# Performance work log

Measured on AMD Instinct MI355X. Metric: run time of the kernel, lower is better.

The kernel has to match this reference:

```python
import jax, jax.numpy as jnp
import numpy as np
from jax import lax

T, B, D, H, K, A = 256, 512, 128, 50, 5, 4


def setup_inputs() -> dict:
    key = jax.random.key(0)
    ks = jax.random.split(key, 12)
    s = 0.05
    return {
        "x": jax.random.normal(ks[0], (T, B, D), dtype=jnp.float32),
        "W_in": jax.random.normal(ks[1], (H, D), dtype=jnp.float32) * s,
        "b_in": jax.random.normal(ks[2], (H,), dtype=jnp.float32) * s,
        "W_ctx": jax.random.normal(ks[3], (H, 2 * H), dtype=jnp.float32) * s,
        "b_ctx": jax.random.normal(ks[4], (H,), dtype=jnp.float32) * s,
        "W_key": jax.random.normal(ks[5], (K, H), dtype=jnp.float32) * s,
        "b_key": jax.random.normal(ks[6], (K,), dtype=jnp.float32) * s,
        "W_q": jax.random.normal(ks[7], (K, H), dtype=jnp.float32) * s,
        "b_q": jax.random.normal(ks[8], (K,), dtype=jnp.float32) * s,
        "first_context": jax.random.normal(ks[9], (H,), dtype=jnp.float32) * s,
        "W_act": jax.random.normal(ks[10], (A, H), dtype=jnp.float32) * s,
        "b_act": jax.random.normal(ks[11], (A,), dtype=jnp.float32) * s,
    }


def reference(x, W_in, b_in, W_ctx, b_ctx, W_key, b_key, W_q, b_q,
              first_context, W_act, b_act):
    # Unrolls the torch module's per-step forward() over T steps with a
    # growing attention context (horizon=-1 => attend to full history).
    Tn, Bn, _ = x.shape
    Hn = W_in.shape[0]
    Kn = W_key.shape[0]
    neg_inf = jnp.float32(-1e30)

    c0 = jnp.broadcast_to(first_context[None, :], (Bn, Hn))  # [B,H]
    ctx_buf = jnp.zeros((Tn + 1, Bn, Hn), x.dtype).at[0].set(c0)
    key_buf = jnp.zeros((Tn + 1, Bn, Kn), x.dtype).at[0].set(c0 @ W_key.T + b_key)
    step_ids = jnp.arange(Tn + 1)[:, None]  # [T+1,1]

    def step(carry, xt):
        ctx_buf, key_buf, prev_c, t = carry
        h = jax.nn.relu(xt @ W_in.T + b_in)                           # [B,H]
        c = jax.nn.relu(jnp.concatenate([prev_c, h], axis=1) @ W_ctx.T + b_ctx)
        ctx_buf = ctx_buf.at[t + 1].set(c)
        key_buf = key_buf.at[t + 1].set(c @ W_key.T + b_key)
        q = c @ W_q.T + b_q                                           # [B,K]
        scores = jnp.einsum('tbk,bk->tb', key_buf, q)                 # [T+1,B]
        scores = jnp.where(step_ids <= t + 1, scores, neg_inf)
        attn = jax.nn.softmax(scores, axis=0)                         # over history
        w = jnp.einsum('tb,tbh->bh', attn, ctx_buf)                   # [B,H]
        actions = w @ W_act.T + b_act                                 # [B,A]
        return (ctx_buf, key_buf, c, t + 1), actions

    _, actions = lax.scan(step, (ctx_buf, key_buf, c0, jnp.int32(0)), x)
    return actions  # [T,B,A]
```

## Files before the change

### kernel.cpp

```cpp
#include <hip/hip_runtime.h>

#define TT 256
#define BB 512
#define DD 128
#define HH 50
#define KK 5
#define AA 4
#define NROW 131072
#define GST 52
#define KQS 260

#define R50(X) X(0) X(1) X(2) X(3) X(4) X(5) X(6) X(7) X(8) X(9) \
  X(10) X(11) X(12) X(13) X(14) X(15) X(16) X(17) X(18) X(19) \
  X(20) X(21) X(22) X(23) X(24) X(25) X(26) X(27) X(28) X(29) \
  X(30) X(31) X(32) X(33) X(34) X(35) X(36) X(37) X(38) X(39) \
  X(40) X(41) X(42) X(43) X(44) X(45) X(46) X(47) X(48) X(49)

typedef _Float16 half4 __attribute__((ext_vector_type(4)));
typedef float f32x4 __attribute__((ext_vector_type(4)));

__global__ void k0_prep(const float* __restrict__ W_in,
                        const float* __restrict__ W_ctx,
                        const float* __restrict__ W_key,
                        const float* __restrict__ W_q,
                        const float* __restrict__ b_key,
                        const float* __restrict__ b_q,
                        float* __restrict__ WHT,
                        float* __restrict__ WK2T, float* __restrict__ bias2) {
  int i = blockIdx.x * 256 + threadIdx.x;
  if (i < HH * 52) {
    int j = i / 52, h = i % 52;
    WHT[i] = (h < HH) ? W_ctx[h * (2 * HH) + HH + j] : 0.f;
  }
  if (i < HH * 64) {
    int j = i >> 6, l = i & 63;
    float v = 0.f;
    if (l < HH) v = W_ctx[l * (2 * HH) + j];
    else if (l < HH + KK) v = W_key[(l - HH) * HH + j];
    else if (l < HH + 2 * KK) v = W_q[(l - HH - KK) * HH + j];
    WK2T[i] = v;
  }
  if (i < 64) {
    float bv = 0.f;
    if (i >= HH && i < HH + KK) bv = b_key[i - HH];
    else if (i >= HH + KK && i < HH + 2 * KK) bv = b_q[i - HH - KK];
    bias2[i] = bv;
  }
}

__global__ __launch_bounds__(256, 2) void k1_mfma(
    const float* __restrict__ x, const float* __restrict__ W_in,
    const float* __restrict__ WHT, const float* __restrict__ b_in,
    const float* __restrict__ b_ctx, float* __restrict__ g) {
  const int lane = threadIdx.x & 63;
  const int wave = threadIdx.x >> 6;
  const int lrow = lane & 15, lgrp = lane >> 4;

#define WA1D(m, kk)                                                     \
  half4 wa1_##m##_##kk;                                                 \
  {                                                                     \
    const int hh = 16 * (m) + lrow;                                     \
    const int j0 = 16 * (kk) + 4 * lgrp;                                \
    const bool v = (hh < HH);                                           \
    const float* p = W_in + (size_t)(v ? hh : 0) * DD + j0;             \
    wa1_##m##_##kk[0] = (_Float16)(v ? p[0] : 0.f);                     \
    wa1_##m##_##kk[1] = (_Float16)(v ? p[1] : 0.f);                     \
    wa1_##m##_##kk[2] = (_Float16)(v ? p[2] : 0.f);                     \
    wa1_##m##_##kk[3] = (_Float16)(v ? p[3] : 0.f);                     \
  }
  WA1D(0, 0) WA1D(0, 1) WA1D(0, 2) WA1D(0, 3)
  WA1D(0, 4) WA1D(0, 5) WA1D(0, 6) WA1D(0, 7)
  WA1D(1, 0) WA1D(1, 1) WA1D(1, 2) WA1D(1, 3)
  WA1D(1, 4) WA1D(1, 5) WA1D(1, 6) WA1D(1, 7)
  WA1D(2, 0) WA1D(2, 1) WA1D(2, 2) WA1D(2, 3)
  WA1D(2, 4) WA1D(2, 5) WA1D(2, 6) WA1D(2, 7)
  WA1D(3, 0) WA1D(3, 1) WA1D(3, 2) WA1D(3, 3)
  WA1D(3, 4) WA1D(3, 5) WA1D(3, 6) WA1D(3, 7)

#define WA2D(m, kk)                                                     \
  half4 wa2_##m##_##kk;                                                 \
  {                                                                     \
    const int gg = 16 * (m) + lrow;                                     \
    const int h0 = 16 * (kk) + 4 * lgrp;                                \
    wa2_##m##_##kk[0] = (_Float16)((gg < HH && h0 + 0 < HH) ? WHT[(h0 + 0) * 52 + gg] : 0.f); \
    wa2_##m##_##kk[1] = (_Float16)((gg < HH && h0 + 1 < HH) ? WHT[(h0 + 1) * 52 + gg] : 0.f); \
    wa2_##m##_##kk[2] = (_Float16)((gg < HH && h0 + 2 < HH) ? WHT[(h0 + 2) * 52 + gg] : 0.f); \
    wa2_##m##_##kk[3] = (_Float16)((gg < HH && h0 + 3 < HH) ? WHT[(h0 + 3) * 52 + gg] : 0.f); \
  }
  WA2D(0, 0) WA2D(0, 1) WA2D(0, 2) WA2D(0, 3)
  WA2D(1, 0) WA2D(1, 1) WA2D(1, 2) WA2D(1, 3)
  WA2D(2, 0) WA2D(2, 1) WA2D(2, 2) WA2D(2, 3)
  WA2D(3, 0) WA2D(3, 1) WA2D(3, 2) WA2D(3, 3)

#define BDEF(m, r)                                                      \
  const float bin_##m##_##r =                                           \
      (16 * (m) + 4 * lgrp + (r) < HH) ? b_in[16 * (m) + 4 * lgrp + (r)] : 0.f; \
  const float bct_##m##_##r =                                           \
      (16 * (m) + 4 * lgrp + (r) < HH) ? b_ctx[16 * (m) + 4 * lgrp + (r)] : 0.f;
  BDEF(0, 0) BDEF(0, 1) BDEF(0, 2) BDEF(0, 3)
  BDEF(1, 0) BDEF(1, 1) BDEF(1, 2) BDEF(1, 3)
  BDEF(2, 0) BDEF(2, 1) BDEF(2, 2) BDEF(2, 3)
  BDEF(3, 0) BDEF(3, 1) BDEF(3, 2) BDEF(3, 3)

  const f32x4 zf = {0.f, 0.f, 0.f, 0.f};

#pragma unroll 1
  for (int it = 0; it < 4; ++it) {
    const int tile = (blockIdx.x * 4 + wave) * 4 + it;
    const int row = tile * 16 + lrow;
    const float* __restrict__ xr = x + (size_t)row * DD + 4 * lgrp;

#define XLD(kk)                                                         \
  half4 xb##kk;                                                         \
  {                                                                     \
    const float4 xv = *reinterpret_cast<const float4*>(xr + 16 * kk);   \
    xb##kk[0] = (_Float16)xv.x;                                         \
    xb##kk[1] = (_Float16)xv.y;                                         \
    xb##kk[2] = (_Float16)xv.z;                                         \
    xb##kk[3] = (_Float16)xv.w;                                         \
  }
    XLD(0) XLD(1) XLD(2) XLD(3) XLD(4) XLD(5) XLD(6) XLD(7)

    f32x4 d10 = zf, d11 = zf, d12 = zf, d13 = zf;
#define MM1(kk)                                                              \
  d10 = __builtin_amdgcn_mfma_f32_16x16x16f16(wa1_0_##kk, xb##kk, d10, 0, 0, 0); \
  d11 = __builtin_amdgcn_mfma_f32_16x16x16f16(wa1_1_##kk, xb##kk, d11, 0, 0, 0); \
  d12 = __builtin_amdgcn_mfma_f32_16x16x16f16(wa1_2_##kk, xb##kk, d12, 0, 0, 0); \
  d13 = __builtin_amdgcn_mfma_f32_16x16x16f16(wa1_3_##kk, xb##kk, d13, 0, 0, 0);
    MM1(0) MM1(1) MM1(2) MM1(3) MM1(4) MM1(5) MM1(6) MM1(7)

#define HBD(k)                                                    \
  half4 hb##k;                                                    \
  hb##k[0] = (_Float16)fmaxf(d1##k[0] + bin_##k##_0, 0.f);        \
  hb##k[1] = (_Float16)fmaxf(d1##k[1] + bin_##k##_1, 0.f);        \
  hb##k[2] = (_Float16)fmaxf(d1##k[2] + bin_##k##_2, 0.f);        \
  hb##k[3] = (_Float16)fmaxf(d1##k[3] + bin_##k##_3, 0.f);
    HBD(0) HBD(1) HBD(2) HBD(3)

    f32x4 d20 = zf, d21 = zf, d22 = zf, d23 = zf;
#define MM2(kk)                                                              \
  d20 = __builtin_amdgcn_mfma_f32_16x16x16f16(wa2_0_##kk, hb##kk, d20, 0, 0, 0); \
  d21 = __builtin_amdgcn_mfma_f32_16x16x16f16(wa2_1_##kk, hb##kk, d21, 0, 0, 0); \
  d22 = __builtin_amdgcn_mfma_f32_16x16x16f16(wa2_2_##kk, hb##kk, d22, 0, 0, 0); \
  d23 = __builtin_amdgcn_mfma_f32_16x16x16f16(wa2_3_##kk, hb##kk, d23, 0, 0, 0);
    MM2(0) MM2(1) MM2(2) MM2(3)

    float* __restrict__ gr =
        g + ((size_t)(row & (BB - 1)) * TT + (row >> 9)) * GST;
    *reinterpret_cast<float4*>(gr + 4 * lgrp) =
        make_float4(d20[0] + bct_0_0, d20[1] + bct_0_1, d20[2] + bct_0_2,
                    d20[3] + bct_0_3);
    *reinterpret_cast<float4*>(gr + 16 + 4 * lgrp) =
        make_float4(d21[0] + bct_1_0, d21[1] + bct_1_1, d21[2] + bct_1_2,
                    d21[3] + bct_1_3);
    *reinterpret_cast<float4*>(gr + 32 + 4 * lgrp) =
        make_float4(d22[0] + bct_2_0, d22[1] + bct_2_1, d22[2] + bct_2_2,
                    d22[3] + bct_2_3);
    if (lgrp == 0) {
      *reinterpret_cast<float4*>(gr + 48) =
          make_float4(d23[0] + bct_3_0, d23[1] + bct_3_1, 0.f, 0.f);
    }
  }
}

__global__ __launch_bounds__(64) void k2_rec(
    const float* __restrict__ g, const float* __restrict__ WK2T,
    const float* __restrict__ bias2, const float* __restrict__ first_context,
    float* __restrict__ ctxg, float* __restrict__ kqg) {
  __shared__ __align__(16) float c_lds[64];
  const int b = blockIdx.x;
  const int lane = threadIdx.x;

#define WDECL(j)                            \
  float w##j = WK2T[(j) * 64 + lane];       \
  asm volatile("" : "+v"(w##j));
  R50(WDECL)
  const float wz = 0.f;
  const float bias = bias2[lane];

  const float c0v = (lane < HH) ? first_context[lane] : 0.f;
  c_lds[lane] = (lane < HH) ? c0v : 0.f;
  if (lane < HH) ctxg[((size_t)b * 257 + 0) * HH + lane] = c0v;

  const int gslot = (lane < GST) ? lane : (GST - 1);
  const float* __restrict__ gbp = g + (size_t)b * TT * GST + gslot;
  float gq0 = gbp[0 * GST];
  float gq1 = gbp[1 * GST];
  float gq2 = gbp[2 * GST];
  float gq3 = gbp[3 * GST];

  const bool iskq = (lane >= HH && lane < HH + 2 * KK);
  float* __restrict__ kqrow =
      kqg + ((size_t)b * 10 + (iskq ? lane - HH : 0)) * KQS;

#define KQ(J, wa, wb, wc, wd)                                            \
  {                                                                      \
    const float4 cq = *reinterpret_cast<const float4*>(&c_lds[J]);       \
    acc0 = fmaf(wa, cq.x, acc0);                                         \
    acc1 = fmaf(wb, cq.y, acc1);                                         \
    acc2 = fmaf(wc, cq.z, acc2);                                         \
    acc3 = fmaf(wd, cq.w, acc3);                                         \
  }
#define DOT50R                                                           \
  float acc0 = 0.f, acc1 = 0.f, acc2 = 0.f, acc3 = 0.f;                  \
  KQ(0, w0, w1, w2, w3) KQ(4, w4, w5, w6, w7)                            \
  KQ(8, w8, w9, w10, w11) KQ(12, w12, w13, w14, w15)                     \
  KQ(16, w16, w17, w18, w19) KQ(20, w20, w21, w22, w23)                  \
  KQ(24, w24, w25, w26, w27) KQ(28, w28, w29, w30, w31)                  \
  KQ(32, w32, w33, w34, w35) KQ(36, w36, w37, w38, w39)                  \
  KQ(40, w40, w41, w42, w43) KQ(44, w44, w45, w46, w47)                  \
  KQ(48, w48, w49, wz, wz)                                               \
  const float acc = (acc0 + acc1) + (acc2 + acc3);

#define BODY(RR, GQ)                                                     \
  {                                                                      \
    const int t = tg4 + RR;                                              \
    DOT50R                                                               \
    kqa##RR = acc + bias;                                                \
    const float cn = fmaxf(acc + GQ, 0.f);                               \
    GQ = gbp[(size_t)min(t + 4, TT - 1) * GST];                          \
    if (lane < HH) {                                                     \
      ctxg[((size_t)b * 257 + (t + 1)) * HH + lane] = cn;                \
      c_lds[lane] = cn;                                                  \
    }                                                                    \
  }

#pragma unroll 1
  for (int tg4 = 0; tg4 < TT; tg4 += 4) {
    float kqa0, kqa1, kqa2, kqa3;
    BODY(0, gq0) BODY(1, gq1) BODY(2, gq2) BODY(3, gq3)
    if (iskq) {
      *reinterpret_cast<float4*>(kqrow + tg4) =
          make_float4(kqa0, kqa1, kqa2, kqa3);
    }
  }

  {
    DOT50R
    if (iskq) kqrow[TT] = acc + bias;
  }
}

__global__ __launch_bounds__(256, 4) void k3_attn(
    const float* __restrict__ ctxg, const float* __restrict__ kqg,
    const float* __restrict__ W_act, const float* __restrict__ b_act,
    float* __restrict__ out) {
  __shared__ __align__(16) float ct[64 * 66];
  __shared__ __align__(16) float k_l[16 * 68];
  __shared__ __align__(16) float o_l[64 * 66];
  __shared__ float su_l[64];

  const int tid = threadIdx.x;
  const int bid = blockIdx.x;
  const int chunk = 3 - (bid >> 9);
  const int b = bid & 511;
  const int tbase = chunk * 64;
  const int nst = min(tbase + 66, 257);
  const int ntiles = (nst + 63) >> 6;
  const int wave = tid >> 6;
  const int lane = tid & 63;
  const int lrow = lane & 15;
  const int lgrp = lane >> 4;
  const int tw = tbase + wave * 16;

  for (int i = tid; i < 11 * 68; i += 256) k_l[5 * 68 + i] = 0.f;

  half4 qf;
#pragma unroll
  for (int i = 0; i < 4; ++i) {
    const int k = 4 * lgrp + i;
    qf[i] = (_Float16)((k < KK)
                           ? kqg[((size_t)b * 10 + 5 + k) * KQS + tw + lrow + 1]
                           : 0.f);
  }

  const f32x4 zf = {0.f, 0.f, 0.f, 0.f};
  f32x4 acc0 = zf, acc1 = zf, acc2 = zf, acc3 = zf;
  float su = 0.f;

#pragma unroll 1
  for (int tile = 0; tile < ntiles; ++tile) {
    __syncthreads();
    {
      const int r = tid >> 2;
      const int c0 = (tid & 3) * 16;
      const int srow = tile * 64 + r;
      const float* src = ctxg + ((size_t)b * 257 + srow) * HH;
      const bool sv = (srow < nst);
#pragma unroll
      for (int u = 0; u < 8; ++u) {
        const int c = c0 + u * 2;
        float2 v = make_float2(0.f, 0.f);
        if (sv && c < HH) v = *reinterpret_cast<const float2*>(src + c);
        *reinterpret_cast<float2*>(&ct[r * 66 + c]) = v;
      }
    }
    {
      for (int i = tid; i < KK * 64; i += 256) {
        const int k = i >> 6, sl = i & 63;
        const int s = tile * 64 + sl;
        k_l[k * 68 + sl] =
            (s <= TT) ? kqg[((size_t)b * 10 + k) * KQS + s] : 0.f;
      }
    }
    __syncthreads();

    if (tile * 64 <= tw + 16) {
#pragma unroll 1
      for (int su16 = 0; su16 < 4; ++su16) {
        const int sb = tile * 64 + su16 * 16;
        if (sb > tw + 16) break;

        half4 kf;
#pragma unroll
        for (int i = 0; i < 4; ++i)
          kf[i] = (_Float16)k_l[(4 * lgrp + i) * 68 + su16 * 16 + lrow];

        const f32x4 sc =
            __builtin_amdgcn_mfma_f32_16x16x16f16(kf, qf, zf, 0, 0, 0);

        half4 pa;
#pragma unroll
        for (int r = 0; r < 4; ++r) {
          const int s = sb + 4 * lgrp + r;
          const float p = (s <= tw + lrow + 1) ? __expf(sc[r]) : 0.f;
          su += p;
          pa[r] = (_Float16)p;
        }

        const int vbase = su16 * 16 + 4 * lgrp;
#define PVHT(HT, ACC)                                                     \
  {                                                                       \
    half4 vf;                                                             \
    vf[0] = (_Float16)ct[(vbase + 0) * 66 + lrow + 16 * HT];              \
    vf[1] = (_Float16)ct[(vbase + 1) * 66 + lrow + 16 * HT];              \
    vf[2] = (_Float16)ct[(vbase + 2) * 66 + lrow + 16 * HT];              \
    vf[3] = (_Float16)ct[(vbase + 3) * 66 + lrow + 16 * HT];              \
    ACC = __builtin_amdgcn_mfma_f32_16x16x16f16(pa, vf, ACC, 0, 0, 0);    \
  }
        PVHT(0, acc0) PVHT(1, acc1) PVHT(2, acc2) PVHT(3, acc3)
      }
    }
  }

  su += __shfl_xor(su, 16, 64);
  su += __shfl_xor(su, 32, 64);
  if (lane < 16) su_l[wave * 16 + lane] = su;

#pragma unroll
  for (int r = 0; r < 4; ++r) {
    const int trow = wave * 16 + 4 * lgrp + r;
    o_l[trow * 66 + lrow + 0] = acc0[r];
    o_l[trow * 66 + lrow + 16] = acc1[r];
    o_l[trow * 66 + lrow + 32] = acc2[r];
    o_l[trow * 66 + lrow + 48] = acc3[r];
  }
  __syncthreads();

  {
    const int tl = tid >> 2;
    const int a = tid & 3;
    const float inv = 1.f / su_l[tl];
    const float* orow = &o_l[tl * 66];
    const float* wrow = W_act + a * HH;
    float s0 = 0.f, s1 = 0.f;
#pragma unroll
    for (int h = 0; h < HH; h += 2) {
      s0 = fmaf(orow[h], wrow[h], s0);
      s1 = fmaf(orow[h + 1], wrow[h + 1], s1);
    }
    out[((size_t)(tbase + tl) * BB + b) * AA + a] =
        fmaf(s0 + s1, inv, b_act[a]);
  }
}

extern "C" void kernel_launch(void* const* d_in, const int* in_sizes, int n_in,
                              void* d_out, int out_size, void* d_ws,
                              size_t ws_size, hipStream_t stream) {
  const float* x = (const float*)d_in[0];
  const float* W_in = (const float*)d_in[1];
  const float* b_in = (const float*)d_in[2];
  const float* W_ctx = (const float*)d_in[3];
  const float* b_ctx = (const float*)d_in[4];
  const float* W_key = (const float*)d_in[5];
  const float* b_key = (const float*)d_in[6];
  const float* W_q = (const float*)d_in[7];
  const float* b_q = (const float*)d_in[8];
  const float* fc = (const float*)d_in[9];
  const float* W_act = (const float*)d_in[10];
  const float* b_act = (const float*)d_in[11];
  float* out = (float*)d_out;
  float* ws = (float*)d_ws;

  float* WHT = ws;
  float* WK2T = ws + 4096;
  float* bias2 = ws + 8128;
  float* g = ws + 8192;
  float* ctxg = g + (size_t)NROW * GST + 64;
  float* kqg = ctxg + (size_t)BB * 257 * HH;

  hipLaunchKernelGGL(k0_prep, dim3(26), dim3(256), 0, stream, W_in, W_ctx,
                     W_key, W_q, b_key, b_q, WHT, WK2T, bias2);
  hipLaunchKernelGGL(k1_mfma, dim3(512), dim3(256), 0, stream, x, W_in, WHT,
                     b_in, b_ctx, g);
  hipLaunchKernelGGL(k2_rec, dim3(512), dim3(64), 0, stream, g, WK2T, bias2,
                     fc, ctxg, kqg);
  hipLaunchKernelGGL(k3_attn, dim3(2048), dim3(256), 0, stream, ctxg, kqg,
                     W_act, b_act, out);
}
```

Before: 151.0 us.

## Store gate preactivations as fp16, pad context rows to 64, deepen prefetch

The first stage now writes its per-step context preactivations as half-precision values in a 64-wide padded layout instead of fp32 with stride 52. This halves the intermediate traffic and lets every lane of the recurrent kernel load without clamping. The recurrence stores contexts in 64-float rows without a lane guard, unrolls eight steps per iteration, and prefetches eight steps ahead to hide global load latency in the serial loop. The attention kernel reads the padded rows. fp16 storage of preactivations reduces precision, and the padded context buffer increases write traffic.

```diff
diff --git a/kernel.cpp b/kernel.cpp
--- a/kernel.cpp
+++ b/kernel.cpp
@@ -7,7 +7,6 @@
 #define KK 5
 #define AA 4
 #define NROW 131072
-#define GST 52
 #define KQS 260
 
 #define R50(X) X(0) X(1) X(2) X(3) X(4) X(5) X(6) X(7) X(8) X(9) \
@@ -51,7 +50,7 @@
 __global__ __launch_bounds__(256, 2) void k1_mfma(
     const float* __restrict__ x, const float* __restrict__ W_in,
     const float* __restrict__ WHT, const float* __restrict__ b_in,
-    const float* __restrict__ b_ctx, float* __restrict__ g) {
+    const float* __restrict__ b_ctx, _Float16* __restrict__ gh) {
   const int lane = threadIdx.x & 63;
   const int wave = threadIdx.x >> 6;
   const int lrow = lane & 15, lgrp = lane >> 4;
@@ -145,28 +144,35 @@
   d23 = __builtin_amdgcn_mfma_f32_16x16x16f16(wa2_3_##kk, hb##kk, d23, 0, 0, 0);
     MM2(0) MM2(1) MM2(2) MM2(3)
 
-    float* __restrict__ gr =
-        g + ((size_t)(row & (BB - 1)) * TT + (row >> 9)) * GST;
-    *reinterpret_cast<float4*>(gr + 4 * lgrp) =
-        make_float4(d20[0] + bct_0_0, d20[1] + bct_0_1, d20[2] + bct_0_2,
-                    d20[3] + bct_0_3);
-    *reinterpret_cast<float4*>(gr + 16 + 4 * lgrp) =
-        make_float4(d21[0] + bct_1_0, d21[1] + bct_1_1, d21[2] + bct_1_2,
-                    d21[3] + bct_1_3);
-    *reinterpret_cast<float4*>(gr + 32 + 4 * lgrp) =
-        make_float4(d22[0] + bct_2_0, d22[1] + bct_2_1, d22[2] + bct_2_2,
-                    d22[3] + bct_2_3);
-    if (lgrp == 0) {
-      *reinterpret_cast<float4*>(gr + 48) =
-          make_float4(d23[0] + bct_3_0, d23[1] + bct_3_1, 0.f, 0.f);
+    _Float16* __restrict__ gr =
+        gh + ((size_t)(row & (BB - 1)) * TT + (row >> 9)) * 64;
+#define GST4(off, D, B0, B1, B2, B3)                          \
+  {                                                           \
+    half4 v;                                                  \
+    v[0] = (_Float16)(D[0] + B0);                             \
+    v[1] = (_Float16)(D[1] + B1);                             \
+    v[2] = (_Float16)(D[2] + B2);                             \
+    v[3] = (_Float16)(D[3] + B3);                             \
+    *reinterpret_cast<half4*>(gr + (off) + 4 * lgrp) = v;     \
+  }
+    GST4(0, d20, bct_0_0, bct_0_1, bct_0_2, bct_0_3)
+    GST4(16, d21, bct_1_0, bct_1_1, bct_1_2, bct_1_3)
+    GST4(32, d22, bct_2_0, bct_2_1, bct_2_2, bct_2_3)
+    {
+      half4 v;
+      v[0] = (_Float16)((lgrp == 0) ? d23[0] + bct_3_0 : 0.f);
+      v[1] = (_Float16)((lgrp == 0) ? d23[1] + bct_3_1 : 0.f);
+      v[2] = (_Float16)0.f;
+      v[3] = (_Float16)0.f;
+      *reinterpret_cast<half4*>(gr + 48 + 4 * lgrp) = v;
     }
   }
 }
 
 __global__ __launch_bounds__(64) void k2_rec(
-    const float* __restrict__ g, const float* __restrict__ WK2T,
+    const _Float16* __restrict__ gh, const float* __restrict__ WK2T,
     const float* __restrict__ bias2, const float* __restrict__ first_context,
-    float* __restrict__ ctxg, float* __restrict__ kqg) {
+    float* __restrict__ ctxg64, float* __restrict__ kqg) {
   __shared__ __align__(16) float c_lds[64];
   const int b = blockIdx.x;
   const int lane = threadIdx.x;
@@ -179,16 +185,20 @@
   const float bias = bias2[lane];
 
   const float c0v = (lane < HH) ? first_context[lane] : 0.f;
-  c_lds[lane] = (lane < HH) ? c0v : 0.f;
-  if (lane < HH) ctxg[((size_t)b * 257 + 0) * HH + lane] = c0v;
-
-  const int gslot = (lane < GST) ? lane : (GST - 1);
-  const float* __restrict__ gbp = g + (size_t)b * TT * GST + gslot;
-  float gq0 = gbp[0 * GST];
-  float gq1 = gbp[1 * GST];
-  float gq2 = gbp[2 * GST];
-  float gq3 = gbp[3 * GST];
-
+  c_lds[lane] = c0v;
+  ctxg64[((size_t)b * 257 + 0) * 64 + lane] = c0v;
+
+  const _Float16* __restrict__ gbp = gh + (size_t)b * TT * 64 + lane;
+  float gq0 = (float)gbp[0 * 64];
+  float gq1 = (float)gbp[1 * 64];
+  float gq2 = (float)gbp[2 * 64];
+  float gq3 = (float)gbp[3 * 64];
+  float gq4 = (float)gbp[4 * 64];
+  float gq5 = (float)gbp[5 * 64];
+  float gq6 = (float)gbp[6 * 64];
+  float gq7 = (float)gbp[7 * 64];
+
+  float* __restrict__ ctp = ctxg64 + (size_t)b * 257 * 64 + lane;
   const bool iskq = (lane >= HH && lane < HH + 2 * KK);
   float* __restrict__ kqrow =
       kqg + ((size_t)b * 10 + (iskq ? lane - HH : 0)) * KQS;
@@ -214,24 +224,25 @@
 
 #define BODY(RR, GQ)                                                     \
   {                                                                      \
-    const int t = tg4 + RR;                                              \
+    const int t = tg8 + RR;                                              \
     DOT50R                                                               \
     kqa##RR = acc + bias;                                                \
     const float cn = fmaxf(acc + GQ, 0.f);                               \
-    GQ = gbp[(size_t)min(t + 4, TT - 1) * GST];                          \
-    if (lane < HH) {                                                     \
-      ctxg[((size_t)b * 257 + (t + 1)) * HH + lane] = cn;                \
-      c_lds[lane] = cn;                                                  \
-    }                                                                    \
+    GQ = (float)gbp[(size_t)min(t + 8, TT - 1) * 64];                    \
+    ctp[(size_t)(t + 1) * 64] = cn;                                      \
+    c_lds[lane] = cn;           \
   }
 
 #pragma unroll 1
-  for (int tg4 = 0; tg4 < TT; tg4 += 4) {
-    float kqa0, kqa1, kqa2, kqa3;
+  for (int tg8 = 0; tg8 < TT; tg8 += 8) {
+    float kqa0, kqa1, kqa2, kqa3, kqa4, kqa5, kqa6, kqa7;
     BODY(0, gq0) BODY(1, gq1) BODY(2, gq2) BODY(3, gq3)
+    BODY(4, gq4) BODY(5, gq5) BODY(6, gq6) BODY(7, gq7)
     if (iskq) {
-      *reinterpret_cast<float4*>(kqrow + tg4) =
+      *reinterpret_cast<float4*>(kqrow + tg8) =
           make_float4(kqa0, kqa1, kqa2, kqa3);
+      *reinterpret_cast<float4*>(kqrow + tg8 + 4) =
+          make_float4(kqa4, kqa5, kqa6, kqa7);
     }
   }
 
@@ -242,7 +253,7 @@
 }
 
 __global__ __launch_bounds__(256, 4) void k3_attn(
-    const float* __restrict__ ctxg, const float* __restrict__ kqg,
+    const float* __restrict__ ctxg64, const float* __restrict__ kqg,
     const float* __restrict__ W_act, const float* __restrict__ b_act,
     float* __restrict__ out) {
   __shared__ __align__(16) float ct[64 * 66];
@@ -285,7 +296,7 @@
       const int r = tid >> 2;
       const int c0 = (tid & 3) * 16;
       const int srow = tile * 64 + r;
-      const float* src = ctxg + ((size_t)b * 257 + srow) * HH;
+      const float* src = ctxg64 + ((size_t)b * 257 + srow) * 64;
       const bool sv = (srow < nst);
 #pragma unroll
       for (int u = 0; u < 8; ++u) {
@@ -395,16 +406,16 @@
   float* WHT = ws;
   float* WK2T = ws + 4096;
   float* bias2 = ws + 8128;
-  float* g = ws + 8192;
-  float* ctxg = g + (size_t)NROW * GST + 64;
-  float* kqg = ctxg + (size_t)BB * 257 * HH;
+  _Float16* gh = (_Float16*)(ws + 8192);
+  float* ctxg64 = ws + 8192 + 4194304;
+  float* kqg = ctxg64 + (size_t)BB * 257 * 64;
 
   hipLaunchKernelGGL(k0_prep, dim3(26), dim3(256), 0, stream, W_in, W_ctx,
                      W_key, W_q, b_key, b_q, WHT, WK2T, bias2);
   hipLaunchKernelGGL(k1_mfma, dim3(512), dim3(256), 0, stream, x, W_in, WHT,
-                     b_in, b_ctx, g);
-  hipLaunchKernelGGL(k2_rec, dim3(512), dim3(64), 0, stream, g, WK2T, bias2,
-                     fc, ctxg, kqg);
-  hipLaunchKernelGGL(k3_attn, dim3(2048), dim3(256), 0, stream, ctxg, kqg,
+                     b_in, b_ctx, gh);
+  hipLaunchKernelGGL(k2_rec, dim3(512), dim3(64), 0, stream, gh, WK2T, bias2,
+                     fc, ctxg64, kqg);
+  hipLaunchKernelGGL(k3_attn, dim3(2048), dim3(256), 0, stream, ctxg64, kqg,
                      W_act, b_act, out);
 }
```

Result: slower. 161.2 us (+6.7%).

## Fuse recurrence and attention kernels with LDS producer-consumer waves

Applied to the files above, without the earlier changes.

Merges the sequential context recurrence and the attention/action kernels into a single block per batch element. One wave runs the recurrence and writes contexts and keys/queries as fp16 into LDS, publishing its progress through a shared counter. The other three waves poll that counter and compute attention for 16-step tiles as soon as their history is ready. The action projection is now done in registers with shuffle reductions. This removes the global round trip of ctx/kq, one launch, and overlaps attention with the recurrence. In exchange it uses spin-wait synchronisation without barriers and gives only 512 blocks of 4 waves, which limits occupancy.

```diff
diff --git a/kernel.cpp b/kernel.cpp
--- a/kernel.cpp
+++ b/kernel.cpp
@@ -8,7 +8,8 @@
 #define AA 4
 #define NROW 131072
 #define GST 52
-#define KQS 260
+#define CXS 66
+#define KQR2 18
 
 #define R50(X) X(0) X(1) X(2) X(3) X(4) X(5) X(6) X(7) X(8) X(9) \
   X(10) X(11) X(12) X(13) X(14) X(15) X(16) X(17) X(18) X(19) \
@@ -163,35 +164,44 @@
   }
 }
 
-__global__ __launch_bounds__(64) void k2_rec(
+__global__ __launch_bounds__(256, 2) void k23_fused(
     const float* __restrict__ g, const float* __restrict__ WK2T,
-    const float* __restrict__ bias2, const float* __restrict__ first_context,
-    float* __restrict__ ctxg, float* __restrict__ kqg) {
+    const float* __restrict__ bias2, const float* __restrict__ fc,
+    const float* __restrict__ W_act, const float* __restrict__ b_act,
+    float* __restrict__ out) {
+  __shared__ _Float16 ctx_l[272 * CXS];
+  __shared__ _Float16 kq_l[272 * KQR2];
   __shared__ __align__(16) float c_lds[64];
+  __shared__ int prog;
+
+  const int tid = threadIdx.x;
   const int b = blockIdx.x;
-  const int lane = threadIdx.x;
-
+  const int wv = tid >> 6;
+  const int lane = tid & 63;
+
+  for (int i = tid; i < 272 * CXS; i += 256) ctx_l[i] = (_Float16)0.f;
+  for (int i = tid; i < 272 * KQR2; i += 256) kq_l[i] = (_Float16)0.f;
+  if (tid == 0) prog = 0;
+  __syncthreads();
+
+  if (wv == 0) {
 #define WDECL(j)                            \
   float w##j = WK2T[(j) * 64 + lane];       \
   asm volatile("" : "+v"(w##j));
-  R50(WDECL)
-  const float wz = 0.f;
-  const float bias = bias2[lane];
-
-  const float c0v = (lane < HH) ? first_context[lane] : 0.f;
-  c_lds[lane] = (lane < HH) ? c0v : 0.f;
-  if (lane < HH) ctxg[((size_t)b * 257 + 0) * HH + lane] = c0v;
-
-  const int gslot = (lane < GST) ? lane : (GST - 1);
-  const float* __restrict__ gbp = g + (size_t)b * TT * GST + gslot;
-  float gq0 = gbp[0 * GST];
-  float gq1 = gbp[1 * GST];
-  float gq2 = gbp[2 * GST];
-  float gq3 = gbp[3 * GST];
-
-  const bool iskq = (lane >= HH && lane < HH + 2 * KK);
-  float* __restrict__ kqrow =
-      kqg + ((size_t)b * 10 + (iskq ? lane - HH : 0)) * KQS;
+    R50(WDECL)
+    const float wz = 0.f;
+    const float bias = bias2[lane];
+
+    const float c0v = (lane < HH) ? fc[lane] : 0.f;
+    c_lds[lane] = (lane < HH) ? c0v : 0.f;
+    if (lane < HH) ctx_l[0 * CXS + lane] = (_Float16)c0v;
+
+    const int gslot = (lane < GST) ? lane : (GST - 1);
+    const float* __restrict__ gbp = g + (size_t)b * TT * GST + gslot;
+    float gq0 = gbp[0 * GST];
+    float gq1 = gbp[1 * GST];
+    float gq2 = gbp[2 * GST];
+    float gq3 = gbp[3 * GST];
 
 #define KQ(J, wa, wb, wc, wd)                                            \
   {                                                                      \
@@ -212,109 +222,73 @@
   KQ(48, w48, w49, wz, wz)                                               \
   const float acc = (acc0 + acc1) + (acc2 + acc3);
 
-#define BODY(RR, GQ)                                                     \
+#define BODYF(RR, GQ)                                                    \
   {                                                                      \
     const int t = tg4 + RR;                                              \
     DOT50R                                                               \
-    kqa##RR = acc + bias;                                                \
+    if (lane >= HH) kq_l[t * KQR2 + (lane - HH)] = (_Float16)(acc + bias); \
     const float cn = fmaxf(acc + GQ, 0.f);                               \
     GQ = gbp[(size_t)min(t + 4, TT - 1) * GST];                          \
     if (lane < HH) {                                                     \
-      ctxg[((size_t)b * 257 + (t + 1)) * HH + lane] = cn;                \
+      ctx_l[(t + 1) * CXS + lane] = (_Float16)cn;                        \
       c_lds[lane] = cn;                                                  \
     }                                                                    \
   }
 
 #pragma unroll 1
-  for (int tg4 = 0; tg4 < TT; tg4 += 4) {
-    float kqa0, kqa1, kqa2, kqa3;
-    BODY(0, gq0) BODY(1, gq1) BODY(2, gq2) BODY(3, gq3)
-    if (iskq) {
-      *reinterpret_cast<float4*>(kqrow + tg4) =
-          make_float4(kqa0, kqa1, kqa2, kqa3);
-    }
-  }
-
-  {
-    DOT50R
-    if (iskq) kqrow[TT] = acc + bias;
-  }
-}
-
-__global__ __launch_bounds__(256, 4) void k3_attn(
-    const float* __restrict__ ctxg, const float* __restrict__ kqg,
-    const float* __restrict__ W_act, const float* __restrict__ b_act,
-    float* __restrict__ out) {
-  __shared__ __align__(16) float ct[64 * 66];
-  __shared__ __align__(16) float k_l[16 * 68];
-  __shared__ __align__(16) float o_l[64 * 66];
-  __shared__ float su_l[64];
-
-  const int tid = threadIdx.x;
-  const int bid = blockIdx.x;
-  const int chunk = 3 - (bid >> 9);
-  const int b = bid & 511;
-  const int tbase = chunk * 64;
-  const int nst = min(tbase + 66, 257);
-  const int ntiles = (nst + 63) >> 6;
-  const int wave = tid >> 6;
-  const int lane = tid & 63;
-  const int lrow = lane & 15;
-  const int lgrp = lane >> 4;
-  const int tw = tbase + wave * 16;
-
-  for (int i = tid; i < 11 * 68; i += 256) k_l[5 * 68 + i] = 0.f;
-
-  half4 qf;
-#pragma unroll
-  for (int i = 0; i < 4; ++i) {
-    const int k = 4 * lgrp + i;
-    qf[i] = (_Float16)((k < KK)
-                           ? kqg[((size_t)b * 10 + 5 + k) * KQS + tw + lrow + 1]
-                           : 0.f);
-  }
-
-  const f32x4 zf = {0.f, 0.f, 0.f, 0.f};
-  f32x4 acc0 = zf, acc1 = zf, acc2 = zf, acc3 = zf;
-  float su = 0.f;
-
-#pragma unroll 1
-  for (int tile = 0; tile < ntiles; ++tile) {
-    __syncthreads();
-    {
-      const int r = tid >> 2;
-      const int c0 = (tid & 3) * 16;
-      const int srow = tile * 64 + r;
-      const float* src = ctxg + ((size_t)b * 257 + srow) * HH;
-      const bool sv = (srow < nst);
-#pragma unroll
-      for (int u = 0; u < 8; ++u) {
-        const int c = c0 + u * 2;
-        float2 v = make_float2(0.f, 0.f);
-        if (sv && c < HH) v = *reinterpret_cast<const float2*>(src + c);
-        *reinterpret_cast<float2*>(&ct[r * 66 + c]) = v;
+    for (int tg4 = 0; tg4 < TT; tg4 += 4) {
+      BODYF(0, gq0) BODYF(1, gq1) BODYF(2, gq2) BODYF(3, gq3)
+      if ((tg4 & 12) == 12) {
+        asm volatile("" ::: "memory");
+        if (lane == 0) *((volatile int*)&prog) = tg4 + 4;
       }
     }
+
     {
-      for (int i = tid; i < KK * 64; i += 256) {
-        const int k = i >> 6, sl = i & 63;
-        const int s = tile * 64 + sl;
-        k_l[k * 68 + sl] =
-            (s <= TT) ? kqg[((size_t)b * 10 + k) * KQS + s] : 0.f;
+      DOT50R
+      if (lane >= HH) kq_l[TT * KQR2 + (lane - HH)] = (_Float16)(acc + bias);
+    }
+    asm volatile("" ::: "memory");
+    if (lane == 0) *((volatile int*)&prog) = 257;
+
+  } else {
+    const int lrow = lane & 15, lgrp = lane >> 4;
+    const f32x4 zf = {0.f, 0.f, 0.f, 0.f};
+
+#define WACT(a, ht)                                                     \
+  const float wa_##a##_##ht =                                           \
+      (lrow + 16 * (ht) < HH) ? W_act[(a)*HH + lrow + 16 * (ht)] : 0.f;
+    WACT(0, 0) WACT(0, 1) WACT(0, 2) WACT(0, 3)
+    WACT(1, 0) WACT(1, 1) WACT(1, 2) WACT(1, 3)
+    WACT(2, 0) WACT(2, 1) WACT(2, 2) WACT(2, 3)
+    WACT(3, 0) WACT(3, 1) WACT(3, 2) WACT(3, 3)
+    const float ba0 = b_act[0], ba1 = b_act[1];
+    const float ba2 = b_act[2], ba3 = b_act[3];
+
+#pragma unroll 1
+    for (int k = wv - 1; k < 16; k += 3) {
+      const int tw = k * 16;
+      const int need = (tw + 17 > 257) ? 257 : (tw + 17);
+      while (*((volatile int*)&prog) < need) __builtin_amdgcn_s_sleep(8);
+      asm volatile("" ::: "memory");
+
+      half4 qf;
+#pragma unroll
+      for (int i = 0; i < 4; ++i) {
+        const int kk = 4 * lgrp + i;
+        qf[i] = (kk < KK) ? kq_l[(tw + lrow + 1) * KQR2 + 5 + kk]
+                          : (_Float16)0.f;
       }
-    }
-    __syncthreads();
-
-    if (tile * 64 <= tw + 16) {
+
+      f32x4 oa0 = zf, oa1 = zf, oa2 = zf, oa3 = zf;
+      float su = 0.f;
+
 #pragma unroll 1
-      for (int su16 = 0; su16 < 4; ++su16) {
-        const int sb = tile * 64 + su16 * 16;
-        if (sb > tw + 16) break;
-
+      for (int sb = 0; sb <= tw + 16; sb += 16) {
         half4 kf;
 #pragma unroll
         for (int i = 0; i < 4; ++i)
-          kf[i] = (_Float16)k_l[(4 * lgrp + i) * 68 + su16 * 16 + lrow];
+          kf[i] = kq_l[(sb + lrow) * KQR2 + 4 * lgrp + i];
 
         const f32x4 sc =
             __builtin_amdgcn_mfma_f32_16x16x16f16(kf, qf, zf, 0, 0, 0);
@@ -328,49 +302,55 @@
           pa[r] = (_Float16)p;
         }
 
-        const int vbase = su16 * 16 + 4 * lgrp;
-#define PVHT(HT, ACC)                                                     \
+        const int vb = sb + 4 * lgrp;
+#define PVF(HT, ACC)                                                      \
   {                                                                       \
     half4 vf;                                                             \
-    vf[0] = (_Float16)ct[(vbase + 0) * 66 + lrow + 16 * HT];              \
-    vf[1] = (_Float16)ct[(vbase + 1) * 66 + lrow + 16 * HT];              \
-    vf[2] = (_Float16)ct[(vbase + 2) * 66 + lrow + 16 * HT];              \
-    vf[3] = (_Float16)ct[(vbase + 3) * 66 + lrow + 16 * HT];              \
+    vf[0] = ctx_l[(vb + 0) * CXS + lrow + 16 * HT];                       \
+    vf[1] = ctx_l[(vb + 1) * CXS + lrow + 16 * HT];                       \
+    vf[2] = ctx_l[(vb + 2) * CXS + lrow + 16 * HT];                       \
+    vf[3] = ctx_l[(vb + 3) * CXS + lrow + 16 * HT];                       \
     ACC = __builtin_amdgcn_mfma_f32_16x16x16f16(pa, vf, ACC, 0, 0, 0);    \
   }
-        PVHT(0, acc0) PVHT(1, acc1) PVHT(2, acc2) PVHT(3, acc3)
+        PVF(0, oa0) PVF(1, oa1) PVF(2, oa2) PVF(3, oa3)
       }
+
+      su += __shfl_xor(su, 16, 64);
+      su += __shfl_xor(su, 32, 64);
+
+#define PTC(r)                                                                 \
+  float pt##r##_0 = oa0[r] * wa_0_0 + oa1[r] * wa_0_1 + oa2[r] * wa_0_2 +      \
+                    oa3[r] * wa_0_3;                                           \
+  float pt##r##_1 = oa0[r] * wa_1_0 + oa1[r] * wa_1_1 + oa2[r] * wa_1_2 +      \
+                    oa3[r] * wa_1_3;                                           \
+  float pt##r##_2 = oa0[r] * wa_2_0 + oa1[r] * wa_2_1 + oa2[r] * wa_2_2 +      \
+                    oa3[r] * wa_2_3;                                           \
+  float pt##r##_3 = oa0[r] * wa_3_0 + oa1[r] * wa_3_1 + oa2[r] * wa_3_2 +      \
+                    oa3[r] * wa_3_3;
+      PTC(0) PTC(1) PTC(2) PTC(3)
+#define REDX(v)                 \
+  v += __shfl_xor(v, 1, 64);    \
+  v += __shfl_xor(v, 2, 64);    \
+  v += __shfl_xor(v, 4, 64);    \
+  v += __shfl_xor(v, 8, 64);
+      REDX(pt0_0) REDX(pt0_1) REDX(pt0_2) REDX(pt0_3)
+      REDX(pt1_0) REDX(pt1_1) REDX(pt1_2) REDX(pt1_3)
+      REDX(pt2_0) REDX(pt2_1) REDX(pt2_2) REDX(pt2_3)
+      REDX(pt3_0) REDX(pt3_1) REDX(pt3_2) REDX(pt3_3)
+
+#define EPI(r)                                                            \
+  {                                                                       \
+    const float sur = __shfl(su, 4 * lgrp + (r), 64);                     \
+    if (lrow == 0) {                                                      \
+      const float inv = 1.f / sur;                                        \
+      const int t = tw + 4 * lgrp + (r);                                  \
+      *reinterpret_cast<float4*>(out + ((size_t)t * BB + b) * AA) =       \
+          make_float4(fmaf(pt##r##_0, inv, ba0), fmaf(pt##r##_1, inv, ba1), \
+                      fmaf(pt##r##_2, inv, ba2), fmaf(pt##r##_3, inv, ba3)); \
+    }                                                                     \
+  }
+      EPI(0) EPI(1) EPI(2) EPI(3)
     }
-  }
-
-  su += __shfl_xor(su, 16, 64);
-  su += __shfl_xor(su, 32, 64);
-  if (lane < 16) su_l[wave * 16 + lane] = su;
-
-#pragma unroll
-  for (int r = 0; r < 4; ++r) {
-    const int trow = wave * 16 + 4 * lgrp + r;
-    o_l[trow * 66 + lrow + 0] = acc0[r];
-    o_l[trow * 66 + lrow + 16] = acc1[r];
-    o_l[trow * 66 + lrow + 32] = acc2[r];
-    o_l[trow * 66 + lrow + 48] = acc3[r];
-  }
-  __syncthreads();
-
-  {
-    const int tl = tid >> 2;
-    const int a = tid & 3;
-    const float inv = 1.f / su_l[tl];
-    const float* orow = &o_l[tl * 66];
-    const float* wrow = W_act + a * HH;
-    float s0 = 0.f, s1 = 0.f;
-#pragma unroll
-    for (int h = 0; h < HH; h += 2) {
-      s0 = fmaf(orow[h], wrow[h], s0);
-      s1 = fmaf(orow[h + 1], wrow[h + 1], s1);
-    }
-    out[((size_t)(tbase + tl) * BB + b) * AA + a] =
-        fmaf(s0 + s1, inv, b_act[a]);
   }
 }
 
@@ -396,15 +376,11 @@
   float* WK2T = ws + 4096;
   float* bias2 = ws + 8128;
   float* g = ws + 8192;
-  float* ctxg = g + (size_t)NROW * GST + 64;
-  float* kqg = ctxg + (size_t)BB * 257 * HH;
 
   hipLaunchKernelGGL(k0_prep, dim3(26), dim3(256), 0, stream, W_in, W_ctx,
                      W_key, W_q, b_key, b_q, WHT, WK2T, bias2);
   hipLaunchKernelGGL(k1_mfma, dim3(512), dim3(256), 0, stream, x, W_in, WHT,
                      b_in, b_ctx, g);
-  hipLaunchKernelGGL(k2_rec, dim3(512), dim3(64), 0, stream, g, WK2T, bias2,
-                     fc, ctxg, kqg);
-  hipLaunchKernelGGL(k3_attn, dim3(2048), dim3(256), 0, stream, ctxg, kqg,
-                     W_act, b_act, out);
+  hipLaunchKernelGGL(k23_fused, dim3(512), dim3(256), 0, stream, g, WK2T,
+                     bias2, fc, W_act, b_act, out);
 }
```

Result: faster. 145.0 us (-3.9%).
